# Kernel tuning notes

Hardware: AMD Instinct MI355X
Metric: run time of the kernel (lower is better)

## Reference

```python
import jax, jax.numpy as jnp
import numpy as np

TAU = 0.07
EPS = 1e-12  # F.normalize eps


def _l2norm(x):
    n = jnp.sqrt(jnp.sum(x * x, axis=-1, keepdims=True))
    return x / jnp.maximum(n, EPS)


def setup_inputs() -> dict:
    key = jax.random.key(0)
    k1, k2 = jax.random.split(key)
    n_e, e_dim = 4096, 64
    z = jax.random.normal(k1, (8, e_dim, 64, 64), dtype=jnp.float32)
    # embedding initialized uniform(-1/n_e, 1/n_e) in the module
    embedding = jax.random.uniform(k2, (n_e, e_dim), dtype=jnp.float32,
                                   minval=-1.0 / n_e, maxval=1.0 / n_e)
    return {"z": z, "embedding": embedding}


def reference(z, embedding):
    # z: [b, c, h, w] -> [b, h, w, c]
    b, c, h, w = z.shape
    z_bhwc = jnp.transpose(z.astype(jnp.float32), (0, 2, 3, 1))
    z_flat = _l2norm(z_bhwc.reshape(-1, c))          # [N, d]
    emb = _l2norm(embedding)                          # [n_e, d]
    logits = jnp.einsum('bd,nd->bn', z_flat, emb)     # [N, n_e]
    probs = jax.nn.softmax(logits / TAU, axis=-1)
    z_q_flat = probs @ emb                            # [N, d]
    z_q = _l2norm(z_q_flat.reshape(b, h, w, c))
    indices = jnp.argmax(probs, axis=-1)              # [N]
    entropy_loss = jnp.asarray(0.0, dtype=jnp.float32)  # eval mode
    z_q = jnp.transpose(z_q, (0, 3, 1, 2))            # back to [b, c, h, w]
    return (z_q, entropy_loss, indices)
```

## Files before the change

kernel.cpp:

```cpp
#include <hip/hip_runtime.h>
#include <hip/hip_bf16.h>

typedef unsigned short u16;
typedef unsigned int u32;
typedef __attribute__((ext_vector_type(4))) float f32x4;
typedef __attribute__((ext_vector_type(16))) float f32x16;
typedef __attribute__((ext_vector_type(4))) u32 u32x4;
typedef __attribute__((ext_vector_type(8))) __bf16 bf16x8;

#define LAM 20.60992915555662f

__device__ __forceinline__ void gl16(const void* g, void* l) {
  __builtin_amdgcn_global_load_lds(
      (const __attribute__((address_space(1))) unsigned int*)g,
      (__attribute__((address_space(3))) unsigned int*)l, 16, 0, 0);
}

__device__ __forceinline__ u32 cvtpk(float a, float b) {
  u32 r;
  asm("v_cvt_pk_bf16_f32 %0, %1, %2" : "=v"(r) : "v"(a), "v"(b));
  return r;
}

__device__ __forceinline__ float exp2a(float x) {
  float r;
  asm("v_exp_f32 %0, %1" : "=v"(r) : "v"(x));
  return r;
}

__device__ __forceinline__ u32 umaxu(u32 a, u32 b) { return a > b ? a : b; }
__device__ __forceinline__ u32 uminu(u32 a, u32 b) { return a < b ? a : b; }

__global__ __launch_bounds__(256) void k_prep(
    const float* __restrict__ emb, const float* __restrict__ z,
    float* __restrict__ einv, u16* __restrict__ ehi, u16* __restrict__ elo,
    u16* __restrict__ et, u16* __restrict__ zhi, u16* __restrict__ zlo,
    float* __restrict__ out) {
  __shared__ union {
    u16 ehl[64][72];
    float zt[64][65];
  } sm;
  const int bx = blockIdx.x, t = threadIdx.x;
  if (bx < 64) {
    const int ch = bx;
    const int e = t >> 2, q = t & 3;
    const int ge = ch * 64 + e;
    float v[16];
#pragma unroll
    for (int b = 0; b < 4; b++)
      *reinterpret_cast<float4*>(v + 4 * b) =
          *reinterpret_cast<const float4*>(emb + (size_t)ge * 64 + q * 16 + 4 * b);
    float ss = 0.f;
#pragma unroll
    for (int j = 0; j < 16; j++) ss += v[j] * v[j];
    ss += __shfl_xor(ss, 1);
    ss += __shfl_xor(ss, 2);
    float inv = 1.0f / fmaxf(sqrtf(ss), 1e-12f);
    if (q == 0) einv[ge] = inv;
    u16 hi[16], lo[16];
#pragma unroll
    for (int j = 0; j < 16; j++) {
      float n = v[j] * inv;
      __bf16 h = (__bf16)n;
      hi[j] = __builtin_bit_cast(u16, h);
      __bf16 l = (__bf16)(n - (float)h);
      lo[j] = __builtin_bit_cast(u16, l);
    }
#pragma unroll
    for (int bb = 0; bb < 2; bb++) {
      int b = 2 * q + bb;
      int pos = (b ^ (e & 7)) * 8;
      *reinterpret_cast<uint4*>(ehi + (size_t)ge * 64 + pos) =
          *reinterpret_cast<const uint4*>(hi + 8 * bb);
      *reinterpret_cast<uint4*>(elo + (size_t)ge * 64 + pos) =
          *reinterpret_cast<const uint4*>(lo + 8 * bb);
    }
    *reinterpret_cast<uint4*>(&sm.ehl[e][q * 16]) = *reinterpret_cast<const uint4*>(hi);
    *reinterpret_cast<uint4*>(&sm.ehl[e][q * 16 + 8]) = *reinterpret_cast<const uint4*>(hi + 8);
    __syncthreads();
    {
      const int d = t >> 2, eq = t & 3;
      u16 vals[16];
#pragma unroll
      for (int j = 0; j < 16; j++) vals[j] = sm.ehl[eq * 16 + j][d];
#pragma unroll
      for (int bb = 0; bb < 2; bb++) {
        int b = 2 * eq + bb;
        int pos = (b ^ (d & 7)) * 8;
        *reinterpret_cast<uint4*>(et + (size_t)ch * 4096 + d * 64 + pos) =
            *reinterpret_cast<const uint4*>(vals + 8 * bb);
      }
    }
    if (ch == 0 && t == 0) out[2097152] = 0.0f;
  } else {
    const int p0 = (bx - 64) * 64;
    const float* zb = z + (size_t)(p0 >> 12) * 262144 + (p0 & 4095);
#pragma unroll
    for (int k = 0; k < 4; k++) {
      int idx = k * 1024 + t * 4;
      int c = idx >> 6, px = idx & 63;
      float4 v = *reinterpret_cast<const float4*>(zb + (size_t)c * 4096 + px);
      sm.zt[c][px] = v.x; sm.zt[c][px + 1] = v.y; sm.zt[c][px + 2] = v.z; sm.zt[c][px + 3] = v.w;
    }
    __syncthreads();
    const int px = t >> 2, cq = t & 3;
    float ss = 0.f;
#pragma unroll
    for (int j = 0; j < 16; j++) { float v = sm.zt[cq * 16 + j][px]; ss += v * v; }
    ss += __shfl_xor(ss, 1);
    ss += __shfl_xor(ss, 2);
    float inv = 1.0f / fmaxf(sqrtf(ss), 1e-12f);
    const int p = p0 + px;
#pragma unroll
    for (int j0 = 0; j0 < 16; j0 += 4) {
      u16 hs[4], ls[4];
#pragma unroll
      for (int j = 0; j < 4; j++) {
        float n = sm.zt[cq * 16 + j0 + j][px] * inv;
        __bf16 h = (__bf16)n;
        hs[j] = __builtin_bit_cast(u16, h);
        __bf16 l = (__bf16)(n - (float)h);
        ls[j] = __builtin_bit_cast(u16, l);
      }
      *reinterpret_cast<ushort4*>(zhi + (size_t)p * 64 + cq * 16 + j0) = make_ushort4(hs[0], hs[1], hs[2], hs[3]);
      *reinterpret_cast<ushort4*>(zlo + (size_t)p * 64 + cq * 16 + j0) = make_ushort4(ls[0], ls[1], ls[2], ls[3]);
    }
  }
}

__global__ __launch_bounds__(256, 4) void k_main(
    const u16* __restrict__ zhi, const u16* __restrict__ zlo,
    const u16* __restrict__ ehi, const u16* __restrict__ elo,
    const u16* __restrict__ et, float* __restrict__ Osum,
    u32* __restrict__ pk1, u32* __restrict__ pk2) {
  __shared__ __align__(16) u16 sA[2][2][4096];
  __shared__ __align__(16) u16 sV[4096];
  const int t = threadIdx.x;
  const int w = t >> 6, lane = t & 63;
  const int H = lane >> 5, c = lane & 31;
  const int bx = blockIdx.x;
  const int s = bx >> 8, tile = bx & 255;
  const int px = tile * 128 + w * 32 + c;

  bf16x8 qh[4], ql[4];
#pragma unroll
  for (int kc = 0; kc < 4; kc++) {
    qh[kc] = *reinterpret_cast<const bf16x8*>(zhi + (size_t)px * 64 + kc * 16 + H * 8);
    ql[kc] = *reinterpret_cast<const bf16x8*>(zlo + (size_t)px * 64 + kc * 16 + H * 8);
  }

  int cb[4];
#pragma unroll
  for (int kc = 0; kc < 4; kc++) cb[kc] = 8 * ((2 * kc + H) ^ (c & 7));
  const int row0 = c * 64, row1 = (32 + c) * 64;

  f32x16 O0 = (f32x16)(0.0f), O1 = (f32x16)(0.0f);
  u32 p1 = 0u, p2 = 0u;
  const u32 vH4 = (u32)(4 * H);

  {
    const size_t gb = (size_t)(s * 16) * 4096;
#pragma unroll
    for (int u = 0; u < 2; u++) {
      int off = t * 8 + u * 2048;
      gl16(ehi + gb + off, &sA[0][0][off]);
      gl16(elo + gb + off, &sA[0][1][off]);
    }
  }
  __syncthreads();

  for (int ch = 0; ch < 16; ch++) {
    const int cur = ch & 1;
    {
      const size_t gv = (size_t)(s * 16 + ch) * 4096;
#pragma unroll
      for (int u = 0; u < 2; u++) {
        int off = t * 8 + u * 2048;
        gl16(et + gv + off, &sV[off]);
      }
    }
    if (ch + 1 < 16) {
      const size_t gb = (size_t)(s * 16 + ch + 1) * 4096;
#pragma unroll
      for (int u = 0; u < 2; u++) {
        int off = t * 8 + u * 2048;
        gl16(ehi + gb + off, &sA[cur ^ 1][0][off]);
        gl16(elo + gb + off, &sA[cur ^ 1][1][off]);
      }
    }
    const u16* sh = sA[cur][0];
    const u16* sl = sA[cur][1];

    f32x16 sa0, sa1;
    {
      f32x16 acc = (f32x16)(0.0f);
#pragma unroll
      for (int kc = 0; kc < 4; kc++) {
        bf16x8 ah = *reinterpret_cast<const bf16x8*>(&sh[row0 + cb[kc]]);
        bf16x8 al = *reinterpret_cast<const bf16x8*>(&sl[row0 + cb[kc]]);
        acc = __builtin_amdgcn_mfma_f32_32x32x16_bf16(ah, qh[kc], acc, 0, 0, 0);
        acc = __builtin_amdgcn_mfma_f32_32x32x16_bf16(al, qh[kc], acc, 0, 0, 0);
        acc = __builtin_amdgcn_mfma_f32_32x32x16_bf16(ah, ql[kc], acc, 0, 0, 0);
      }
      sa0 = acc;
    }
    {
      f32x16 acc = (f32x16)(0.0f);
#pragma unroll
      for (int kc = 0; kc < 4; kc++) {
        bf16x8 ah = *reinterpret_cast<const bf16x8*>(&sh[row1 + cb[kc]]);
        bf16x8 al = *reinterpret_cast<const bf16x8*>(&sl[row1 + cb[kc]]);
        acc = __builtin_amdgcn_mfma_f32_32x32x16_bf16(ah, qh[kc], acc, 0, 0, 0);
        acc = __builtin_amdgcn_mfma_f32_32x32x16_bf16(al, qh[kc], acc, 0, 0, 0);
        acc = __builtin_amdgcn_mfma_f32_32x32x16_bf16(ah, ql[kc], acc, 0, 0, 0);
      }
      sa1 = acc;
    }

    const int e0 = (s * 16 + ch) * 64;
    u32 pk[2][8];
#pragma unroll
    for (int nt = 0; nt < 2; nt++) {
      float pe[16];
#pragma unroll
      for (int reg = 0; reg < 16; reg++) {
        float svv = nt ? sa1[reg] : sa0[reg];
        u32 tfix = (u32)fmaf(svv, 262144.0f, 524288.0f);
        u32 pckd = (tfix << 12) |
                   ((u32)(e0 + nt * 32 + (reg & 3) + 8 * (reg >> 2)) | vH4);
        p2 = umaxu(p2, uminu(pckd, p1));
        p1 = umaxu(p1, pckd);
        pe[reg] = exp2a(fmaf(svv, LAM, -LAM));
      }
#pragma unroll
      for (int qq = 0; qq < 8; qq++) pk[nt][qq] = cvtpk(pe[2 * qq], pe[2 * qq + 1]);
    }

    __syncthreads();

#pragma unroll
    for (int km = 0; km < 4; km++) {
      const int nt = km >> 1, m1 = km & 1;
      u32 ax = pk[nt][4 * m1 + 0], bx2 = pk[nt][4 * m1 + 2];
      u32 ay = pk[nt][4 * m1 + 1], by2 = pk[nt][4 * m1 + 3];
      asm("v_permlane32_swap_b32 %0, %1" : "+v"(ax), "+v"(bx2));
      asm("v_permlane32_swap_b32 %0, %1" : "+v"(ay), "+v"(by2));
      u32x4 bv; bv.x = ax; bv.y = ay; bv.z = bx2; bv.w = by2;
      bf16x8 pb = __builtin_bit_cast(bf16x8, bv);
      bf16x8 a0 = *reinterpret_cast<const bf16x8*>(&sV[row0 + cb[km]]);
      bf16x8 a1 = *reinterpret_cast<const bf16x8*>(&sV[row1 + cb[km]]);
      O0 = __builtin_amdgcn_mfma_f32_32x32x16_bf16(a0, pb, O0, 0, 0, 0);
      O1 = __builtin_amdgcn_mfma_f32_32x32x16_bf16(a1, pb, O1, 0, 0, 0);
    }
    __syncthreads();
  }

  {
    u32 o1 = (u32)__shfl_xor((int)p1, 32);
    u32 o2 = (u32)__shfl_xor((int)p2, 32);
    u32 n1 = umaxu(p1, o1);
    u32 n2 = umaxu(uminu(p1, o1), umaxu(p2, o2));
    if (H == 0) {
      int o = s * 32768 + px;
      pk1[o] = n1;
      pk2[o] = n2;
    }
  }
#pragma unroll
  for (int reg = 0; reg < 16; reg++) {
    int d0 = (reg & 3) + 8 * (reg >> 2) + 4 * H;
    unsafeAtomicAdd(&Osum[(size_t)d0 * 32768 + px], O0[reg]);
    unsafeAtomicAdd(&Osum[(size_t)(d0 + 32) * 32768 + px], O1[reg]);
  }
}

__global__ __launch_bounds__(256) void k_combine(
    const float* __restrict__ Osum, const u32* __restrict__ pk1,
    const u32* __restrict__ pk2, const float* __restrict__ z,
    const float* __restrict__ emb, const float* __restrict__ einv,
    float* __restrict__ out) {
  const int t = threadIdx.x;
  const int pxl = t >> 2, part = t & 3;
  const int px = blockIdx.x * 64 + pxl;
  const int b_ = px >> 12, hw = px & 4095;

  float v[16];
#pragma unroll
  for (int j = 0; j < 16; j++) v[j] = Osum[(size_t)(part * 16 + j) * 32768 + px];
  float ss = 0.f;
#pragma unroll
  for (int j = 0; j < 16; j++) ss = fmaf(v[j], v[j], ss);
  ss += __shfl_xor(ss, 1);
  ss += __shfl_xor(ss, 2);
  float inv = 1.0f / fmaxf(sqrtf(ss), 1e-30f);
#pragma unroll
  for (int j = 0; j < 16; j++)
    out[(size_t)b_ * 262144 + (size_t)(part * 16 + j) * 4096 + hw] = v[j] * inv;

  u32 m1 = pk1[px], m2 = pk2[px];
#pragma unroll
  for (int sg = 1; sg < 4; sg++) {
    u32 a1 = pk1[sg * 32768 + px], a2 = pk2[sg * 32768 + px];
    u32 t2 = umaxu(umaxu(m2, a2), uminu(m1, a1));
    m1 = umaxu(m1, a1);
    m2 = t2;
  }
  const int j1 = (int)(m1 & 0xFFFu), j2 = (int)(m2 & 0xFFFu);

  {
    const float* zc = z + (size_t)b_ * 262144 + (size_t)(part * 16) * 4096 + hw;
    const float* e1 = emb + (size_t)j1 * 64 + part * 16;
    const float* e2 = emb + (size_t)j2 * 64 + part * 16;
    double d1 = 0.0, d2 = 0.0;
#pragma unroll
    for (int j = 0; j < 16; j++) {
      double zv = (double)zc[(size_t)j * 4096];
      d1 += zv * (double)e1[j];
      d2 += zv * (double)e2[j];
    }
    d1 += __shfl_xor(d1, 1); d1 += __shfl_xor(d1, 2);
    d2 += __shfl_xor(d2, 1); d2 += __shfl_xor(d2, 2);
    d1 *= (double)einv[j1];
    d2 *= (double)einv[j2];
    if (part == 0) {
      int best = (d2 > d1 || (d2 == d1 && j2 < j1)) ? j2 : j1;
      out[2097153 + px] = (float)best;
    }
  }
}

extern "C" void kernel_launch(void* const* d_in, const int* in_sizes, int n_in,
                              void* d_out, int out_size, void* d_ws, size_t ws_size,
                              hipStream_t stream) {
  const float* z = (const float*)d_in[0];
  const float* emb = (const float*)d_in[1];
  float* out = (float*)d_out;
  char* ws = (char*)d_ws;
  float* Osum = (float*)(ws + 0);
  u32*   pk1  = (u32*)(ws + 8388608);
  u32*   pk2  = (u32*)(ws + 8912896);
  u16*   zhi  = (u16*)(ws + 9437184);
  u16*   zlo  = (u16*)(ws + 13631488);
  u16*   ehi  = (u16*)(ws + 17825792);
  u16*   elo  = (u16*)(ws + 18350080);
  u16*   et   = (u16*)(ws + 18874368);
  float* einv = (float*)(ws + 19398656);

  hipMemsetAsync(Osum, 0, 8388608, stream);
  k_prep<<<dim3(576), dim3(256), 0, stream>>>(emb, z, einv, ehi, elo, et, zhi, zlo, out);
  k_main<<<dim3(1024), dim3(256), 0, stream>>>(zhi, zlo, ehi, elo, et, Osum, pk1, pk2);
  k_combine<<<dim3(512), dim3(256), 0, stream>>>(Osum, pk1, pk2, z, emb, einv, out);
}
```

Before: 170.2 us.

## Fuse z normalization into main kernel and finalize tiles via last-block counter

The z prep stage moves into k_main: each wave loads its z pixels through LDS, normalizes them and splits them into bf16 hi/lo in registers, so the zhi/zlo buffers are no longer written or read. The separate combine kernel is replaced by an atomic per-tile counter. The last of the four codebook-split blocks for a tile reads Osum and the packed argmax candidates, then writes the normalized output and the indices. This saves a kernel launch and a global round trip, at the cost of a serialized tail inside the last block and extra work in k_main.

```diff
diff --git a/kernel.cpp b/kernel.cpp
--- a/kernel.cpp
+++ b/kernel.cpp
@@ -31,123 +31,131 @@
 __device__ __forceinline__ u32 umaxu(u32 a, u32 b) { return a > b ? a : b; }
 __device__ __forceinline__ u32 uminu(u32 a, u32 b) { return a < b ? a : b; }
 
-__global__ __launch_bounds__(256) void k_prep(
-    const float* __restrict__ emb, const float* __restrict__ z,
-    float* __restrict__ einv, u16* __restrict__ ehi, u16* __restrict__ elo,
-    u16* __restrict__ et, u16* __restrict__ zhi, u16* __restrict__ zlo,
+__device__ __forceinline__ float ALf(const float* p) {
+  return __hip_atomic_load(p, __ATOMIC_RELAXED, __HIP_MEMORY_SCOPE_AGENT);
+}
+__device__ __forceinline__ u32 ALu(const u32* p) {
+  return __hip_atomic_load(p, __ATOMIC_RELAXED, __HIP_MEMORY_SCOPE_AGENT);
+}
+
+__global__ __launch_bounds__(256) void k_eprep(
+    const float* __restrict__ emb, float* __restrict__ einv,
+    u16* __restrict__ ehi, u16* __restrict__ elo, u16* __restrict__ et,
     float* __restrict__ out) {
-  __shared__ union {
-    u16 ehl[64][72];
-    float zt[64][65];
-  } sm;
-  const int bx = blockIdx.x, t = threadIdx.x;
-  if (bx < 64) {
-    const int ch = bx;
-    const int e = t >> 2, q = t & 3;
-    const int ge = ch * 64 + e;
-    float v[16];
-#pragma unroll
-    for (int b = 0; b < 4; b++)
-      *reinterpret_cast<float4*>(v + 4 * b) =
-          *reinterpret_cast<const float4*>(emb + (size_t)ge * 64 + q * 16 + 4 * b);
-    float ss = 0.f;
-#pragma unroll
-    for (int j = 0; j < 16; j++) ss += v[j] * v[j];
-    ss += __shfl_xor(ss, 1);
-    ss += __shfl_xor(ss, 2);
-    float inv = 1.0f / fmaxf(sqrtf(ss), 1e-12f);
-    if (q == 0) einv[ge] = inv;
-    u16 hi[16], lo[16];
-#pragma unroll
-    for (int j = 0; j < 16; j++) {
-      float n = v[j] * inv;
-      __bf16 h = (__bf16)n;
-      hi[j] = __builtin_bit_cast(u16, h);
-      __bf16 l = (__bf16)(n - (float)h);
-      lo[j] = __builtin_bit_cast(u16, l);
-    }
+  __shared__ u16 ehl[64][72];
+  const int ch = blockIdx.x, t = threadIdx.x;
+  const int e = t >> 2, q = t & 3;
+  const int ge = ch * 64 + e;
+  float v[16];
+#pragma unroll
+  for (int b = 0; b < 4; b++)
+    *reinterpret_cast<float4*>(v + 4 * b) =
+        *reinterpret_cast<const float4*>(emb + (size_t)ge * 64 + q * 16 + 4 * b);
+  float ss = 0.f;
+#pragma unroll
+  for (int j = 0; j < 16; j++) ss += v[j] * v[j];
+  ss += __shfl_xor(ss, 1);
+  ss += __shfl_xor(ss, 2);
+  float inv = 1.0f / fmaxf(sqrtf(ss), 1e-12f);
+  if (q == 0) einv[ge] = inv;
+  u16 hi[16], lo[16];
+#pragma unroll
+  for (int j = 0; j < 16; j++) {
+    float n = v[j] * inv;
+    __bf16 h = (__bf16)n;
+    hi[j] = __builtin_bit_cast(u16, h);
+    __bf16 l = (__bf16)(n - (float)h);
+    lo[j] = __builtin_bit_cast(u16, l);
+  }
+#pragma unroll
+  for (int bb = 0; bb < 2; bb++) {
+    int b = 2 * q + bb;
+    int pos = (b ^ (e & 7)) * 8;
+    *reinterpret_cast<uint4*>(ehi + (size_t)ge * 64 + pos) =
+        *reinterpret_cast<const uint4*>(hi + 8 * bb);
+    *reinterpret_cast<uint4*>(elo + (size_t)ge * 64 + pos) =
+        *reinterpret_cast<const uint4*>(lo + 8 * bb);
+  }
+  *reinterpret_cast<uint4*>(&ehl[e][q * 16]) = *reinterpret_cast<const uint4*>(hi);
+  *reinterpret_cast<uint4*>(&ehl[e][q * 16 + 8]) = *reinterpret_cast<const uint4*>(hi + 8);
+  __syncthreads();
+  {
+    const int d = t >> 2, eq = t & 3;
+    u16 vals[16];
+#pragma unroll
+    for (int j = 0; j < 16; j++) vals[j] = ehl[eq * 16 + j][d];
 #pragma unroll
     for (int bb = 0; bb < 2; bb++) {
-      int b = 2 * q + bb;
-      int pos = (b ^ (e & 7)) * 8;
-      *reinterpret_cast<uint4*>(ehi + (size_t)ge * 64 + pos) =
-          *reinterpret_cast<const uint4*>(hi + 8 * bb);
-      *reinterpret_cast<uint4*>(elo + (size_t)ge * 64 + pos) =
-          *reinterpret_cast<const uint4*>(lo + 8 * bb);
-    }
-    *reinterpret_cast<uint4*>(&sm.ehl[e][q * 16]) = *reinterpret_cast<const uint4*>(hi);
-    *reinterpret_cast<uint4*>(&sm.ehl[e][q * 16 + 8]) = *reinterpret_cast<const uint4*>(hi + 8);
-    __syncthreads();
-    {
-      const int d = t >> 2, eq = t & 3;
-      u16 vals[16];
-#pragma unroll
-      for (int j = 0; j < 16; j++) vals[j] = sm.ehl[eq * 16 + j][d];
-#pragma unroll
-      for (int bb = 0; bb < 2; bb++) {
-        int b = 2 * eq + bb;
-        int pos = (b ^ (d & 7)) * 8;
-        *reinterpret_cast<uint4*>(et + (size_t)ch * 4096 + d * 64 + pos) =
-            *reinterpret_cast<const uint4*>(vals + 8 * bb);
-      }
-    }
-    if (ch == 0 && t == 0) out[2097152] = 0.0f;
-  } else {
-    const int p0 = (bx - 64) * 64;
-    const float* zb = z + (size_t)(p0 >> 12) * 262144 + (p0 & 4095);
-#pragma unroll
-    for (int k = 0; k < 4; k++) {
-      int idx = k * 1024 + t * 4;
-      int c = idx >> 6, px = idx & 63;
-      float4 v = *reinterpret_cast<const float4*>(zb + (size_t)c * 4096 + px);
-      sm.zt[c][px] = v.x; sm.zt[c][px + 1] = v.y; sm.zt[c][px + 2] = v.z; sm.zt[c][px + 3] = v.w;
-    }
-    __syncthreads();
-    const int px = t >> 2, cq = t & 3;
-    float ss = 0.f;
-#pragma unroll
-    for (int j = 0; j < 16; j++) { float v = sm.zt[cq * 16 + j][px]; ss += v * v; }
-    ss += __shfl_xor(ss, 1);
-    ss += __shfl_xor(ss, 2);
-    float inv = 1.0f / fmaxf(sqrtf(ss), 1e-12f);
-    const int p = p0 + px;
-#pragma unroll
-    for (int j0 = 0; j0 < 16; j0 += 4) {
-      u16 hs[4], ls[4];
-#pragma unroll
-      for (int j = 0; j < 4; j++) {
-        float n = sm.zt[cq * 16 + j0 + j][px] * inv;
-        __bf16 h = (__bf16)n;
-        hs[j] = __builtin_bit_cast(u16, h);
-        __bf16 l = (__bf16)(n - (float)h);
-        ls[j] = __builtin_bit_cast(u16, l);
-      }
-      *reinterpret_cast<ushort4*>(zhi + (size_t)p * 64 + cq * 16 + j0) = make_ushort4(hs[0], hs[1], hs[2], hs[3]);
-      *reinterpret_cast<ushort4*>(zlo + (size_t)p * 64 + cq * 16 + j0) = make_ushort4(ls[0], ls[1], ls[2], ls[3]);
-    }
-  }
+      int b = 2 * eq + bb;
+      int pos = (b ^ (d & 7)) * 8;
+      *reinterpret_cast<uint4*>(et + (size_t)ch * 4096 + d * 64 + pos) =
+          *reinterpret_cast<const uint4*>(vals + 8 * bb);
+    }
+  }
+  if (ch == 0 && t == 0) out[2097152] = 0.0f;
 }
 
 __global__ __launch_bounds__(256, 4) void k_main(
-    const u16* __restrict__ zhi, const u16* __restrict__ zlo,
+    const float* __restrict__ z, const float* __restrict__ emb,
+    const float* __restrict__ einv,
     const u16* __restrict__ ehi, const u16* __restrict__ elo,
     const u16* __restrict__ et, float* __restrict__ Osum,
-    u32* __restrict__ pk1, u32* __restrict__ pk2) {
-  __shared__ __align__(16) u16 sA[2][2][4096];
-  __shared__ __align__(16) u16 sV[4096];
+    u32* __restrict__ pk1, u32* __restrict__ pk2, int* __restrict__ cnt,
+    float* __restrict__ out) {
+  __shared__ __align__(16) union SM {
+    struct { u16 A[2][2][4096]; u16 V[4096]; } m;
+    float ztr[4][2304];
+    struct { float olds[64][128]; float part[2][128]; float inv[128]; } f;
+  } sm;
+  __shared__ int lastf;
+
   const int t = threadIdx.x;
   const int w = t >> 6, lane = t & 63;
   const int H = lane >> 5, c = lane & 31;
   const int bx = blockIdx.x;
   const int s = bx >> 8, tile = bx & 255;
-  const int px = tile * 128 + w * 32 + c;
+  const int px0g = tile * 128;
+  const int px = px0g + w * 32 + c;
+  const int b_ = px0g >> 12, hw0 = px0g & 4095;
 
   bf16x8 qh[4], ql[4];
-#pragma unroll
-  for (int kc = 0; kc < 4; kc++) {
-    qh[kc] = *reinterpret_cast<const bf16x8*>(zhi + (size_t)px * 64 + kc * 16 + H * 8);
-    ql[kc] = *reinterpret_cast<const bf16x8*>(zlo + (size_t)px * 64 + kc * 16 + H * 8);
-  }
+  {
+    float* zt = &sm.ztr[w][0];
+    const float* zb = z + (size_t)b_ * 262144 + hw0 + w * 32;
+#pragma unroll
+    for (int i = 0; i < 8; i++) {
+      int cc = i * 8 + (lane >> 3), col4 = (lane & 7) * 4;
+      float4 v = *reinterpret_cast<const float4*>(zb + (size_t)cc * 4096 + col4);
+      *reinterpret_cast<float4*>(zt + cc * 36 + col4) = v;
+    }
+    const int cpx = lane & 31;
+    float val[4][8];
+    float ss = 0.f;
+#pragma unroll
+    for (int kc = 0; kc < 4; kc++)
+#pragma unroll
+      for (int j = 0; j < 8; j++) {
+        float vv = zt[(kc * 16 + 8 * H + j) * 36 + cpx];
+        val[kc][j] = vv;
+        ss = fmaf(vv, vv, ss);
+      }
+    ss += __shfl_xor(ss, 32);
+    float inv = 1.0f / fmaxf(sqrtf(ss), 1e-12f);
+#pragma unroll
+    for (int kc = 0; kc < 4; kc++) {
+      bf16x8 xh, xl;
+#pragma unroll
+      for (int j = 0; j < 8; j++) {
+        float n = val[kc][j] * inv;
+        __bf16 h = (__bf16)n;
+        xh[j] = h;
+        xl[j] = (__bf16)(n - (float)h);
+      }
+      qh[kc] = xh;
+      ql[kc] = xl;
+    }
+  }
+  __syncthreads();
 
   int cb[4];
 #pragma unroll
@@ -163,8 +171,8 @@
 #pragma unroll
     for (int u = 0; u < 2; u++) {
       int off = t * 8 + u * 2048;
-      gl16(ehi + gb + off, &sA[0][0][off]);
-      gl16(elo + gb + off, &sA[0][1][off]);
+      gl16(ehi + gb + off, &sm.m.A[0][0][off]);
+      gl16(elo + gb + off, &sm.m.A[0][1][off]);
     }
   }
   __syncthreads();
@@ -176,7 +184,7 @@
 #pragma unroll
       for (int u = 0; u < 2; u++) {
         int off = t * 8 + u * 2048;
-        gl16(et + gv + off, &sV[off]);
+        gl16(et + gv + off, &sm.m.V[off]);
       }
     }
     if (ch + 1 < 16) {
@@ -184,12 +192,12 @@
 #pragma unroll
       for (int u = 0; u < 2; u++) {
         int off = t * 8 + u * 2048;
-        gl16(ehi + gb + off, &sA[cur ^ 1][0][off]);
-        gl16(elo + gb + off, &sA[cur ^ 1][1][off]);
-      }
-    }
-    const u16* sh = sA[cur][0];
-    const u16* sl = sA[cur][1];
+        gl16(ehi + gb + off, &sm.m.A[cur ^ 1][0][off]);
+        gl16(elo + gb + off, &sm.m.A[cur ^ 1][1][off]);
+      }
+    }
+    const u16* sh = sm.m.A[cur][0];
+    const u16* sl = sm.m.A[cur][1];
 
     f32x16 sa0, sa1;
     {
@@ -247,8 +255,8 @@
       asm("v_permlane32_swap_b32 %0, %1" : "+v"(ay), "+v"(by2));
       u32x4 bv; bv.x = ax; bv.y = ay; bv.z = bx2; bv.w = by2;
       bf16x8 pb = __builtin_bit_cast(bf16x8, bv);
-      bf16x8 a0 = *reinterpret_cast<const bf16x8*>(&sV[row0 + cb[km]]);
-      bf16x8 a1 = *reinterpret_cast<const bf16x8*>(&sV[row1 + cb[km]]);
+      bf16x8 a0 = *reinterpret_cast<const bf16x8*>(&sm.m.V[row0 + cb[km]]);
+      bf16x8 a1 = *reinterpret_cast<const bf16x8*>(&sm.m.V[row1 + cb[km]]);
       O0 = __builtin_amdgcn_mfma_f32_32x32x16_bf16(a0, pb, O0, 0, 0, 0);
       O1 = __builtin_amdgcn_mfma_f32_32x32x16_bf16(a1, pb, O1, 0, 0, 0);
     }
@@ -272,59 +280,68 @@
     unsafeAtomicAdd(&Osum[(size_t)d0 * 32768 + px], O0[reg]);
     unsafeAtomicAdd(&Osum[(size_t)(d0 + 32) * 32768 + px], O1[reg]);
   }
-}
-
-__global__ __launch_bounds__(256) void k_combine(
-    const float* __restrict__ Osum, const u32* __restrict__ pk1,
-    const u32* __restrict__ pk2, const float* __restrict__ z,
-    const float* __restrict__ emb, const float* __restrict__ einv,
-    float* __restrict__ out) {
-  const int t = threadIdx.x;
-  const int pxl = t >> 2, part = t & 3;
-  const int px = blockIdx.x * 64 + pxl;
-  const int b_ = px >> 12, hw = px & 4095;
-
-  float v[16];
-#pragma unroll
-  for (int j = 0; j < 16; j++) v[j] = Osum[(size_t)(part * 16 + j) * 32768 + px];
-  float ss = 0.f;
-#pragma unroll
-  for (int j = 0; j < 16; j++) ss = fmaf(v[j], v[j], ss);
-  ss += __shfl_xor(ss, 1);
-  ss += __shfl_xor(ss, 2);
-  float inv = 1.0f / fmaxf(sqrtf(ss), 1e-30f);
-#pragma unroll
-  for (int j = 0; j < 16; j++)
-    out[(size_t)b_ * 262144 + (size_t)(part * 16 + j) * 4096 + hw] = v[j] * inv;
-
-  u32 m1 = pk1[px], m2 = pk2[px];
-#pragma unroll
-  for (int sg = 1; sg < 4; sg++) {
-    u32 a1 = pk1[sg * 32768 + px], a2 = pk2[sg * 32768 + px];
-    u32 t2 = umaxu(umaxu(m2, a2), uminu(m1, a1));
-    m1 = umaxu(m1, a1);
-    m2 = t2;
-  }
-  const int j1 = (int)(m1 & 0xFFFu), j2 = (int)(m2 & 0xFFFu);
-
-  {
-    const float* zc = z + (size_t)b_ * 262144 + (size_t)(part * 16) * 4096 + hw;
-    const float* e1 = emb + (size_t)j1 * 64 + part * 16;
-    const float* e2 = emb + (size_t)j2 * 64 + part * 16;
+
+  __threadfence();
+  __syncthreads();
+  if (t == 0) lastf = atomicAdd(&cnt[tile], 1);
+  __syncthreads();
+  if (lastf != 3) return;
+  __threadfence();
+
+#pragma unroll 4
+  for (int i = 0; i < 32; i++) {
+    int idx = i * 256 + t, d = idx >> 7, pxl = idx & 127;
+    sm.f.olds[d][pxl] = ALf(&Osum[(size_t)d * 32768 + px0g + pxl]);
+  }
+  __syncthreads();
+  {
+    int pxl = t & 127, dh = t >> 7;
+    float ss2 = 0.f;
+#pragma unroll 8
+    for (int dd = 0; dd < 32; dd++) {
+      float v = sm.f.olds[dh * 32 + dd][pxl];
+      ss2 = fmaf(v, v, ss2);
+    }
+    sm.f.part[dh][pxl] = ss2;
+  }
+  __syncthreads();
+  if (t < 128) sm.f.inv[t] = 1.0f / fmaxf(sqrtf(sm.f.part[0][t] + sm.f.part[1][t]), 1e-30f);
+  __syncthreads();
+#pragma unroll 4
+  for (int i = 0; i < 32; i++) {
+    int d = 2 * i + (t >> 7), pxl = t & 127;
+    out[(size_t)b_ * 262144 + (size_t)d * 4096 + hw0 + pxl] = sm.f.olds[d][pxl] * sm.f.inv[pxl];
+  }
+  {
+    const int pxl = t >> 1, half = t & 1;
+    const int gpx = px0g + pxl;
+    u32 m1 = ALu(&pk1[gpx]), m2 = ALu(&pk2[gpx]);
+#pragma unroll
+    for (int sg = 1; sg < 4; sg++) {
+      u32 a1 = ALu(&pk1[sg * 32768 + gpx]), a2 = ALu(&pk2[sg * 32768 + gpx]);
+      u32 t2 = umaxu(umaxu(m2, a2), uminu(m1, a1));
+      m1 = umaxu(m1, a1);
+      m2 = t2;
+    }
+    const int j1 = (int)(m1 & 0xFFFu), j2 = (int)(m2 & 0xFFFu);
+    const float* zc = z + (size_t)b_ * 262144 + hw0 + pxl;
+    const float* e1 = emb + (size_t)j1 * 64;
+    const float* e2 = emb + (size_t)j2 * 64;
     double d1 = 0.0, d2 = 0.0;
-#pragma unroll
-    for (int j = 0; j < 16; j++) {
-      double zv = (double)zc[(size_t)j * 4096];
-      d1 += zv * (double)e1[j];
-      d2 += zv * (double)e2[j];
-    }
-    d1 += __shfl_xor(d1, 1); d1 += __shfl_xor(d1, 2);
-    d2 += __shfl_xor(d2, 1); d2 += __shfl_xor(d2, 2);
+#pragma unroll 8
+    for (int j = 0; j < 32; j++) {
+      int cc = half * 32 + j;
+      double zv = (double)zc[(size_t)cc * 4096];
+      d1 += zv * (double)e1[cc];
+      d2 += zv * (double)e2[cc];
+    }
+    d1 += __shfl_xor(d1, 1);
+    d2 += __shfl_xor(d2, 1);
     d1 *= (double)einv[j1];
     d2 *= (double)einv[j2];
-    if (part == 0) {
+    if (half == 0) {
       int best = (d2 > d1 || (d2 == d1 && j2 < j1)) ? j2 : j1;
-      out[2097153 + px] = (float)best;
+      out[2097153 + gpx] = (float)best;
     }
   }
 }
@@ -337,17 +354,16 @@
   float* out = (float*)d_out;
   char* ws = (char*)d_ws;
   float* Osum = (float*)(ws + 0);
-  u32*   pk1  = (u32*)(ws + 8388608);
-  u32*   pk2  = (u32*)(ws + 8912896);
-  u16*   zhi  = (u16*)(ws + 9437184);
-  u16*   zlo  = (u16*)(ws + 13631488);
-  u16*   ehi  = (u16*)(ws + 17825792);
-  u16*   elo  = (u16*)(ws + 18350080);
-  u16*   et   = (u16*)(ws + 18874368);
-  float* einv = (float*)(ws + 19398656);
-
-  hipMemsetAsync(Osum, 0, 8388608, stream);
-  k_prep<<<dim3(576), dim3(256), 0, stream>>>(emb, z, einv, ehi, elo, et, zhi, zlo, out);
-  k_main<<<dim3(1024), dim3(256), 0, stream>>>(zhi, zlo, ehi, elo, et, Osum, pk1, pk2);
-  k_combine<<<dim3(512), dim3(256), 0, stream>>>(Osum, pk1, pk2, z, emb, einv, out);
-}
+  int*   cnt  = (int*)(ws + 8388608);
+  u32*   pk1  = (u32*)(ws + 8389632);
+  u32*   pk2  = (u32*)(ws + 8913920);
+  u16*   ehi  = (u16*)(ws + 9438208);
+  u16*   elo  = (u16*)(ws + 9962496);
+  u16*   et   = (u16*)(ws + 10486784);
+  float* einv = (float*)(ws + 11011072);
+
+  hipMemsetAsync(ws, 0, 8389632, stream);
+  k_eprep<<<dim3(64), dim3(256), 0, stream>>>(emb, einv, ehi, elo, et, out);
+  k_main<<<dim3(1024), dim3(256), 0, stream>>>(z, emb, einv, ehi, elo, et,
+                                               Osum, pk1, pk2, cnt, out);
+}
```

New measurement: 240.6 us. 1.41x slower.
